# Kernel optimization log

Hardware: AMD Instinct MI355X
Metric: run time of the kernel (lower is better)

Reference implementation:

```python
import jax, jax.numpy as jnp
import numpy as np

N, E_RAND, IN, HID, OUT = 10000, 320000, 512, 256, 256
E = E_RAND + N  # random edges + self loops
TEMP, LAM, LAMBDA_LOSS, BN_EPS = 0.5, 1e-3, 1.0, 1e-5


def _normalize(x):
    # F.normalize: x / max(||x||, 1e-12)
    return x / jnp.maximum(jnp.linalg.norm(x, axis=-1, keepdims=True), 1e-12)


def setup_inputs() -> dict:
    key = jax.random.key(0)
    ks = jax.random.split(key, 12)
    feat = jax.random.normal(ks[0], (N, IN), jnp.float32)
    loops = jnp.arange(N)
    src = jnp.concatenate([jax.random.randint(ks[1], (E_RAND,), 0, N), loops])
    dst = jnp.concatenate([jax.random.randint(ks[2], (E_RAND,), 0, N), loops])
    def lin(k, i, o):
        return jax.random.normal(k, (i, o), jnp.float32) / np.sqrt(i).astype(np.float32)
    return {
        'feat': feat,
        'W1': lin(ks[3], IN, HID), 'b1': jnp.zeros((HID,), jnp.float32),
        'W2': lin(ks[4], HID, OUT), 'b2': jnp.zeros((OUT,), jnp.float32),
        'Wt1': lin(ks[5], IN, HID), 'bt1': jnp.zeros((HID,), jnp.float32),
        'gamma': jnp.ones((HID,), jnp.float32), 'beta': jnp.zeros((HID,), jnp.float32),
        'Wt2': lin(ks[6], HID, OUT), 'bt2': jnp.zeros((OUT,), jnp.float32),
        'Wp': lin(ks[7], HID, HID), 'bp': jnp.zeros((HID,), jnp.float32),
        'src': src, 'dst': dst,
    }


def reference(feat, W1, b1, W2, b2, Wt1, bt1, gamma, beta, Wt2, bt2, Wp, bp, src, dst):
    n = feat.shape[0]
    ones = jnp.ones(src.shape, feat.dtype)
    deg_out = jax.ops.segment_sum(ones, src, num_segments=n)
    deg_in = jax.ops.segment_sum(ones, dst, num_segments=n)
    # symmetric GCN norm per edge (self-loops included so degrees >= 1)
    norm_e = jax.lax.rsqrt(deg_out)[src] * jax.lax.rsqrt(deg_in)[dst]

    def gconv(x, W, b):
        xw = x @ W  # [n, d_out]
        agg = jax.ops.segment_sum(xw[src] * norm_e[:, None], dst, num_segments=n)
        return agg + b

    # GCN encoder (2 layers, no LN)
    h = jax.nn.relu(gconv(feat, W1, b1))
    h = gconv(h, W2, b2)

    # target MLP encoder: linear -> BN(train) -> relu -> linear
    t = feat @ Wt1 + bt1
    mu = t.mean(0)
    var = t.var(0)  # biased, as BatchNorm normalization
    t = (t - mu) * jax.lax.rsqrt(var + BN_EPS) * gamma + beta
    trans = jax.nn.relu(t) @ Wt2 + bt2

    z = _normalize(h)                    # [n, d]
    q = _normalize(trans @ Wp + bp)      # projector (num_MLP=1)

    # pos_score: per-edge sum(z[u]*q[v])/temp, mean over in-edges at v
    sim_e = jnp.einsum('ed,ed->e', z[src], q[dst]) / TEMP
    pos = jax.ops.segment_sum(sim_e, dst, num_segments=n) / deg_in

    # neg_score (neg_sample=0): dense NxN similarity row-sums
    neg_sim = jnp.exp(z @ z.T / TEMP).sum(1)           # per-node
    neg_sim2 = LAM * jnp.exp(z @ q.T / TEMP).sum(1)    # per-node
    m_e = jnp.log(neg_sim[dst] + neg_sim2[src])
    neg = jax.ops.segment_sum(m_e, dst, num_segments=n) / deg_in

    loss = jnp.mean(-pos + LAMBDA_LOSS * neg)
    return loss
```

## Files before the change

### kernel.cpp

```cpp
#include <hip/hip_runtime.h>
#include <stdint.h>


#define TEMP_INV 2.0f
#define LAMC 1.0e-3f
#define SSCALE 1.6986436f

typedef __attribute__((ext_vector_type(8))) __bf16 bf16x8;
typedef __attribute__((ext_vector_type(4))) float f32x4;

__device__ __forceinline__ unsigned short f2bf(float x) {
  union { float f; unsigned int u; } v; v.f = x;
  unsigned int r = v.u + 0x7FFFu + ((v.u >> 16) & 1u);
  return (unsigned short)(r >> 16);
}

__device__ __forceinline__ void g2lds16(const void* gc, void* l) {
  void* g = const_cast<void*>(gc);
  __builtin_amdgcn_global_load_lds(
      (__attribute__((address_space(1))) void*)g,
      (__attribute__((address_space(3))) void*)l, 16, 0, 0);
}

__global__ void k_deg(const int* __restrict__ src, const int* __restrict__ dst,
                      float* deg_out, float* deg_in, int E) {
  int i = blockIdx.x * blockDim.x + threadIdx.x;
  if (i < E) {
    atomicAdd(&deg_out[src[i]], 1.0f);
    atomicAdd(&deg_in[dst[i]], 1.0f);
  }
}

__global__ void k_rdeg(const float* __restrict__ deg_out, const float* __restrict__ deg_in,
                       float* rdo, float* rdi, float* idi, int N) {
  int i = blockIdx.x * blockDim.x + threadIdx.x;
  if (i < N) {
    float o = deg_out[i], d = deg_in[i];
    rdo[i] = rsqrtf(o);
    rdi[i] = rsqrtf(d);
    idi[i] = 1.0f / d;
  }
}

__global__ void k_scan(const float* __restrict__ deg, int* __restrict__ off, int N, int E) {
  __shared__ int sm[1024];
  int tid = threadIdx.x;
  int chunk = (N + 1023) / 1024;
  int b = tid * chunk;
  int sum = 0;
  for (int j = 0; j < chunk; j++) { int i = b + j; if (i < N) sum += (int)deg[i]; }
  sm[tid] = sum;
  __syncthreads();
  for (int s = 1; s < 1024; s <<= 1) {
    int v = (tid >= s) ? sm[tid - s] : 0;
    __syncthreads();
    sm[tid] += v;
    __syncthreads();
  }
  int run = (tid == 0) ? 0 : sm[tid - 1];
  for (int j = 0; j < chunk; j++) {
    int i = b + j;
    if (i < N) { off[i] = run; run += (int)deg[i]; }
  }
  if (tid == 0) off[N] = E;
}

__global__ void k_fill(const int* __restrict__ src, const int* __restrict__ dst,
                       const int* __restrict__ off, int* cur,
                       const float* __restrict__ rdo, const float* __restrict__ rdi,
                       int* adj, float* aw, int E) {
  int e = blockIdx.x * blockDim.x + threadIdx.x;
  if (e < E) {
    int u = src[e], v = dst[e];
    int slot = off[v] + atomicAdd(&cur[v], 1);
    adj[slot] = u;
    aw[slot] = rdo[u] * rdi[v];
  }
}

template <int K, bool BIAS>
__global__ __launch_bounds__(256, 2) void k_gemmL(const float* A,
                                                  const float* __restrict__ W,
                                                  const float* __restrict__ bias,
                                                  float* C, int M) {
  __shared__ __align__(1024) float Wl[2][32][256];
  const int tid = threadIdx.x;
  const int wv = tid >> 6, ln = tid & 63;
  const int rg = tid >> 4, cg = tid & 15;
  const int row0 = blockIdx.x * 32 + rg * 2;
  const int cb = cg * 4;
  int r0 = row0 < M ? row0 : M - 1;
  int r1 = row0 + 1 < M ? row0 + 1 : M - 1;
  const float* Ar0 = A + (size_t)r0 * K;
  const float* Ar1 = A + (size_t)r1 * K;

  auto STAGE = [&](int k0, int b) {
#pragma unroll
    for (int it = 0; it < 8; it++) {
      int r = it * 4 + wv;
      const float* g = W + (size_t)(k0 + r) * 256 + ln * 4;
      g2lds16(g, (char*)&Wl[b][r][0] + ln * 16);
    }
  };

  constexpr int NC = K / 32;
  STAGE(0, 0);
  float acc[2][16] = {};
  for (int t = 0; t < NC; t++) {
    __syncthreads();
    if (t + 1 < NC) STAGE((t + 1) * 32, (t + 1) & 1);
    const float* Wc = &Wl[t & 1][0][0];
    const int k0 = t * 32;
#pragma unroll
    for (int k4 = 0; k4 < 32; k4 += 4) {
      float4 a0 = *(const float4*)(Ar0 + k0 + k4);
      float4 a1 = *(const float4*)(Ar1 + k0 + k4);
      float a0v[4] = {a0.x, a0.y, a0.z, a0.w};
      float a1v[4] = {a1.x, a1.y, a1.z, a1.w};
#pragma unroll
      for (int i = 0; i < 4; i++) {
#pragma unroll
        for (int tt = 0; tt < 4; tt++) {
          float4 w4 = *(const float4*)(Wc + (k4 + i) * 256 + 64 * tt + cb);
          acc[0][4 * tt + 0] += a0v[i] * w4.x; acc[0][4 * tt + 1] += a0v[i] * w4.y;
          acc[0][4 * tt + 2] += a0v[i] * w4.z; acc[0][4 * tt + 3] += a0v[i] * w4.w;
          acc[1][4 * tt + 0] += a1v[i] * w4.x; acc[1][4 * tt + 1] += a1v[i] * w4.y;
          acc[1][4 * tt + 2] += a1v[i] * w4.z; acc[1][4 * tt + 3] += a1v[i] * w4.w;
        }
      }
    }
  }
#pragma unroll
  for (int r = 0; r < 2; r++) {
    int rr = row0 + r;
    if (rr < M) {
      float* crow = C + (size_t)rr * 256;
#pragma unroll
      for (int tt = 0; tt < 4; tt++) {
        int c = 64 * tt + cb;
        float4 v = {acc[r][4 * tt], acc[r][4 * tt + 1], acc[r][4 * tt + 2], acc[r][4 * tt + 3]};
        if constexpr (BIAS) {
          float4 b4 = *(const float4*)(bias + c);
          v.x += b4.x; v.y += b4.y; v.z += b4.z; v.w += b4.w;
        }
        *(float4*)(crow + c) = v;
      }
    }
  }
}

__global__ void k_bnstat(const float* __restrict__ T, float* s, float* ss, int M) {
  int c = threadIdx.x;
  int r0 = blockIdx.x * 64;
  float a = 0, b = 0;
  for (int r = r0; r < r0 + 64 && r < M; r++) {
    float v = T[(size_t)r * 256 + c];
    a += v; b += v * v;
  }
  atomicAdd(&s[c], a);
  atomicAdd(&ss[c], b);
}

__global__ void k_bnrelu(float* T, const float* __restrict__ s, const float* __restrict__ ss,
                         const float* __restrict__ g, const float* __restrict__ b, int M) {
  int r = blockIdx.x, c = threadIdx.x;
  float invM = 1.0f / (float)M;
  float mu = s[c] * invM;
  float var = ss[c] * invM - mu * mu;
  float w = rsqrtf(var + 1e-5f) * g[c];
  float v = T[(size_t)r * 256 + c];
  v = (v - mu) * w + b[c];
  T[(size_t)r * 256 + c] = fmaxf(v, 0.0f);
}

template <bool UNIT, bool RELU>
__global__ __launch_bounds__(256) void k_agg(const float* __restrict__ X, const int* __restrict__ off,
                                             const int* __restrict__ adj, const float* __restrict__ w,
                                             const float* __restrict__ bias, float* __restrict__ Y, int N) {
  int wv = threadIdx.x >> 6, ln = threadIdx.x & 63;
  int v = blockIdx.x * 4 + wv;
  if (v >= N) return;
  int s0 = off[v], s1 = off[v + 1];
  const float4* X4 = (const float4*)X;
  float4 acc = {0, 0, 0, 0};
  for (int s = s0; s < s1; s++) {
    int u = adj[s];
    float wt = UNIT ? 1.0f : w[s];
    float4 x = X4[(size_t)u * 64 + ln];
    acc.x += wt * x.x; acc.y += wt * x.y; acc.z += wt * x.z; acc.w += wt * x.w;
  }
  if constexpr (!UNIT) {
    float4 b = ((const float4*)bias)[ln];
    acc.x += b.x; acc.y += b.y; acc.z += b.z; acc.w += b.w;
  }
  if constexpr (RELU) {
    acc.x = fmaxf(acc.x, 0.f); acc.y = fmaxf(acc.y, 0.f);
    acc.z = fmaxf(acc.z, 0.f); acc.w = fmaxf(acc.w, 0.f);
  }
  ((float4*)Y)[(size_t)v * 64 + ln] = acc;
}

__global__ __launch_bounds__(256) void k_norm(float* X, unsigned short* Xb, int N, int NPAD) {
  int wv = threadIdx.x >> 6, ln = threadIdx.x & 63;
  int r = blockIdx.x * 4 + wv;
  if (r >= NPAD) return;
  if (r >= N) {
    ushort4 z = {0, 0, 0, 0};
    ((ushort4*)Xb)[(size_t)r * 64 + ln] = z;
    return;
  }
  float4 x = ((const float4*)X)[(size_t)r * 64 + ln];
  float ss = x.x * x.x + x.y * x.y + x.z * x.z + x.w * x.w;
#pragma unroll
  for (int m = 1; m < 64; m <<= 1) ss += __shfl_xor(ss, m, 64);
  float sc = 1.0f / fmaxf(sqrtf(ss), 1e-12f);
  float4 xn = {x.x * sc, x.y * sc, x.z * sc, x.w * sc};
  ((float4*)X)[(size_t)r * 64 + ln] = xn;
  float bs = sc * SSCALE;
  ushort4 b;
  b.x = f2bf(x.x * bs); b.y = f2bf(x.y * bs);
  b.z = f2bf(x.z * bs); b.w = f2bf(x.w * bs);
  ((ushort4*)Xb)[(size_t)r * 64 + ln] = b;
}

__global__ __launch_bounds__(256, 2) void k_sim(const unsigned short* __restrict__ Zb,
                                                const unsigned short* __restrict__ Qb,
                                                float* __restrict__ S1, float* __restrict__ S2,
                                                int N, int JT, int JS) {
  __shared__ __align__(1024) char LB[2][32768];
  const int tid = threadIdx.x;
  const int wv = tid >> 6, ln = tid & 63;
  const int i0 = blockIdx.x * 256;
  const int wb = wv * 64;

  auto STAGE = [&](int jt, int b) {
    int j0 = jt * 32;
    char* Lb = (char*)LB[b];
#pragma unroll
    for (int it = 0; it < 8; it++) {
      int c = it * 4 + wv;
      int L = c * 1024 + ln * 16;
      int r = L >> 9;
      int o = (L & 511) ^ ((r & 7) << 4);
      const char* g = (r < 32) ? (const char*)Zb + (size_t)(j0 + r) * 512 + o
                               : (const char*)Qb + (size_t)(j0 + r - 32) * 512 + o;
      g2lds16(g, Lb + c * 1024);
    }
  };

  int jt0 = (blockIdx.y * JT) / JS;
  int jt1 = ((blockIdx.y + 1) * JT) / JS;

  STAGE(jt0, 0);

  bf16x8 af[4][8];
#pragma unroll
  for (int rf = 0; rf < 4; rf++) {
    const char* arow = (const char*)(Zb + (size_t)(i0 + wb + rf * 16 + (ln & 15)) * 256);
#pragma unroll
    for (int kk = 0; kk < 8; kk++)
      af[rf][kk] = *(const bf16x8*)(arow + kk * 64 + ((ln >> 4) << 4));
  }

  f32x4 rs[4][2] = {};

  __syncthreads();
  int cur = 0;
  for (int jt = jt0; jt < jt1; jt++) {
    if (jt + 1 < jt1) STAGE(jt + 1, cur ^ 1);
    const char* Lb = (const char*)LB[cur];
#pragma unroll
    for (int m = 0; m < 2; m++) {
      f32x4 acc[4][2] = {};
#pragma unroll
      for (int kk = 0; kk < 8; kk++) {
#pragma unroll
        for (int cf = 0; cf < 2; cf++) {
          int brow = m * 32 + cf * 16 + (ln & 15);
          int o = (kk * 64 + ((ln >> 4) << 4)) ^ ((brow & 7) << 4);
          bf16x8 bb = *(const bf16x8*)(Lb + brow * 512 + o);
#pragma unroll
          for (int rf = 0; rf < 4; rf++)
            acc[rf][cf] = __builtin_amdgcn_mfma_f32_16x16x32_bf16(af[rf][kk], bb, acc[rf][cf], 0, 0, 0);
        }
      }
#pragma unroll
      for (int rf = 0; rf < 4; rf++)
#pragma unroll
        for (int i = 0; i < 4; i++)
          rs[rf][m][i] += exp2f(acc[rf][0][i]) + exp2f(acc[rf][1][i]);
    }
    __syncthreads();
    cur ^= 1;
  }

#pragma unroll
  for (int rf = 0; rf < 4; rf++)
#pragma unroll
    for (int m = 0; m < 2; m++)
#pragma unroll
      for (int i = 0; i < 4; i++) {
        float v = rs[rf][m][i];
        v += __shfl_xor(v, 1, 64);
        v += __shfl_xor(v, 2, 64);
        v += __shfl_xor(v, 4, 64);
        v += __shfl_xor(v, 8, 64);
        if ((ln & 15) == 0) {
          int row = i0 + wb + rf * 16 + ((ln >> 4) << 2) + i;
          if (row < N) atomicAdd(((m == 0) ? S1 : S2) + row, v);
        }
      }
}

__global__ __launch_bounds__(256) void k_final(const float* __restrict__ zsum, const float* __restrict__ q,
                                               const float* __restrict__ S1, const float* __restrict__ S2,
                                               const int* __restrict__ off, const int* __restrict__ adj,
                                               const float* __restrict__ idi, float* __restrict__ out,
                                               int N, float pad) {
  int wv = threadIdx.x >> 6, ln = threadIdx.x & 63;
  int v = blockIdx.x * 4 + wv;
  if (v >= N) return;
  float4 zs = ((const float4*)zsum)[(size_t)v * 64 + ln];
  float4 qv = ((const float4*)q)[(size_t)v * 64 + ln];
  float d = zs.x * qv.x + zs.y * qv.y + zs.z * qv.z + zs.w * qv.w;
  float s1v = S1[v] - pad;
  float lg = 0.0f;
  int e0 = off[v], e1 = off[v + 1];
  for (int s = e0 + ln; s < e1; s += 64) {
    int u = adj[s];
    lg += logf(s1v + LAMC * (S2[u] - pad));
  }
#pragma unroll
  for (int m = 1; m < 64; m <<= 1) {
    d += __shfl_xor(d, m, 64);
    lg += __shfl_xor(lg, m, 64);
  }
  if (ln == 0) {
    float inv = idi[v];
    float posv = d * inv * TEMP_INV;
    float negv = lg * inv;
    atomicAdd(out, (negv - posv) * (1.0f / (float)N));
  }
}

extern "C" void kernel_launch(void* const* d_in, const int* in_sizes, int n_in,
                              void* d_out, int out_size, void* d_ws, size_t ws_size,
                              hipStream_t stream) {
  const float* feat  = (const float*)d_in[0];
  const float* W1    = (const float*)d_in[1];
  const float* b1    = (const float*)d_in[2];
  const float* W2    = (const float*)d_in[3];
  const float* b2    = (const float*)d_in[4];
  const float* Wt1   = (const float*)d_in[5];
  const float* bt1   = (const float*)d_in[6];
  const float* gamma = (const float*)d_in[7];
  const float* beta  = (const float*)d_in[8];
  const float* Wt2   = (const float*)d_in[9];
  const float* bt2   = (const float*)d_in[10];
  const float* Wp    = (const float*)d_in[11];
  const float* bp    = (const float*)d_in[12];
  const int*   src   = (const int*)d_in[13];
  const int*   dst   = (const int*)d_in[14];
  const int N = in_sizes[0] / 512;
  const int E = in_sizes[13];
  const int NTI = (N + 255) / 256, NPAD = NTI * 256, JT = NPAD / 32;
  const int JS = 25;
  const float PADF = (float)(NPAD - N);

  char* p = (char*)d_ws;
  auto alloc = [&](size_t bytes) { char* r = p; p += (bytes + 255) & ~(size_t)255; return r; };
  float* B0 = (float*)alloc((size_t)N * 256 * 4);
  float* B1 = (float*)alloc((size_t)N * 256 * 4);
  float* B2 = (float*)alloc((size_t)N * 256 * 4);
  unsigned short* zb = (unsigned short*)alloc((size_t)NPAD * 256 * 2);
  unsigned short* qb = (unsigned short*)alloc((size_t)NPAD * 256 * 2);
  int*   off = (int*)alloc((size_t)(N + 1) * 4);
  int*   adj = (int*)alloc((size_t)E * 4);
  float* aw  = (float*)alloc((size_t)E * 4);
  char*  zblk = p;
  float* deg_out = (float*)alloc((size_t)N * 4);
  float* deg_in  = (float*)alloc((size_t)N * 4);
  int*   cur     = (int*)alloc((size_t)N * 4);
  float* S1 = (float*)alloc((size_t)N * 4);
  float* S2 = (float*)alloc((size_t)N * 4);
  float* bns  = (float*)alloc(256 * 4);
  float* bnss = (float*)alloc(256 * 4);
  size_t zbytes = (size_t)(p - zblk);
  float* rdo = (float*)alloc((size_t)N * 4);
  float* rdi = (float*)alloc((size_t)N * 4);
  float* idi = (float*)alloc((size_t)N * 4);
  (void)ws_size; (void)n_in; (void)out_size;

  hipMemsetAsync(zblk, 0, zbytes, stream);
  hipMemsetAsync(d_out, 0, 4, stream);

  int gE = (E + 255) / 256, gN = (N + 255) / 256, gb = (N + 31) / 32, gw = (N + 3) / 4;
  k_deg<<<gE, 256, 0, stream>>>(src, dst, deg_out, deg_in, E);
  k_rdeg<<<gN, 256, 0, stream>>>(deg_out, deg_in, rdo, rdi, idi, N);
  k_scan<<<1, 1024, 0, stream>>>(deg_in, off, N, E);
  k_fill<<<gE, 256, 0, stream>>>(src, dst, off, cur, rdo, rdi, adj, aw, E);

  k_gemmL<512, false><<<gb, 256, 0, stream>>>(feat, W1, nullptr, B0, N);
  k_gemmL<512, true ><<<gb, 256, 0, stream>>>(feat, Wt1, bt1, B1, N);
  k_bnstat<<<(N + 63) / 64, 256, 0, stream>>>(B1, bns, bnss, N);
  k_bnrelu<<<N, 256, 0, stream>>>(B1, bns, bnss, gamma, beta, N);
  k_gemmL<256, true ><<<gb, 256, 0, stream>>>(B1, Wt2, bt2, B1, N);
  k_gemmL<256, true ><<<gb, 256, 0, stream>>>(B1, Wp, bp, B1, N);

  k_agg<false, true ><<<gw, 256, 0, stream>>>(B0, off, adj, aw, b1, B2, N);
  k_gemmL<256, false><<<gb, 256, 0, stream>>>(B2, W2, nullptr, B0, N);
  k_agg<false, false><<<gw, 256, 0, stream>>>(B0, off, adj, aw, b2, B2, N);

  int gnp = (NPAD + 3) / 4;
  k_norm<<<gnp, 256, 0, stream>>>(B2, zb, N, NPAD);
  k_norm<<<gnp, 256, 0, stream>>>(B1, qb, N, NPAD);

  dim3 gs(NTI, JS);
  k_sim<<<gs, 256, 0, stream>>>(zb, qb, S1, S2, N, JT, JS);

  k_agg<true, false><<<gw, 256, 0, stream>>>(B2, off, adj, aw, nullptr, B0, N);
  k_final<<<gw, 256, 0, stream>>>(B0, B1, S1, S2, off, adj, idi, (float*)d_out, N, PADF);
}
```

Baseline: 814.0 us.

## Use split-bf16 MFMA for dense GEMMs and column-sliced edge aggregation

Replaces the fp32 FMA GEMM with an MFMA kernel. The kernel splits both A and W into bf16 high and low parts and accumulates three products (hi*hi, lo*hi, hi*lo) to keep near-fp32 accuracy. A new per-call kernel converts each weight matrix into transposed hi/lo bf16 buffers, which adds small extra launches. The sparse aggregation now gives each block a 64-column slice with a 4-way unrolled gather, which raises the number of blocks. It also adds s_setprio around the MFMA loops in k_sim and the new GEMM.

```diff
diff --git a/kernel.cpp b/kernel.cpp
--- a/kernel.cpp
+++ b/kernel.cpp
@@ -7,12 +7,16 @@
 #define SSCALE 1.6986436f
 
 typedef __attribute__((ext_vector_type(8))) __bf16 bf16x8;
+typedef __attribute__((ext_vector_type(8))) unsigned short u16x8;
 typedef __attribute__((ext_vector_type(4))) float f32x4;
 
 __device__ __forceinline__ unsigned short f2bf(float x) {
   union { float f; unsigned int u; } v; v.f = x;
   unsigned int r = v.u + 0x7FFFu + ((v.u >> 16) & 1u);
   return (unsigned short)(r >> 16);
+}
+__device__ __forceinline__ float bf2f(unsigned short h) {
+  union { unsigned int u; float f; } v; v.u = ((unsigned int)h) << 16; return v.f;
 }
 
 __device__ __forceinline__ void g2lds16(const void* gc, void* l) {
@@ -78,72 +82,92 @@
   }
 }
 
+__global__ void k_cvtWt(const float* __restrict__ W, unsigned short* __restrict__ Wth,
+                        unsigned short* __restrict__ Wtl, int K) {
+  int k = blockIdx.x, c = threadIdx.x;
+  float x = W[(size_t)k * 256 + c];
+  unsigned short h = f2bf(x);
+  Wth[(size_t)c * K + k] = h;
+  Wtl[(size_t)c * K + k] = f2bf(x - bf2f(h));
+}
+
 template <int K, bool BIAS>
-__global__ __launch_bounds__(256, 2) void k_gemmL(const float* A,
-                                                  const float* __restrict__ W,
-                                                  const float* __restrict__ bias,
-                                                  float* C, int M) {
-  __shared__ __align__(1024) float Wl[2][32][256];
-  const int tid = threadIdx.x;
-  const int wv = tid >> 6, ln = tid & 63;
-  const int rg = tid >> 4, cg = tid & 15;
-  const int row0 = blockIdx.x * 32 + rg * 2;
-  const int cb = cg * 4;
-  int r0 = row0 < M ? row0 : M - 1;
-  int r1 = row0 + 1 < M ? row0 + 1 : M - 1;
-  const float* Ar0 = A + (size_t)r0 * K;
-  const float* Ar1 = A + (size_t)r1 * K;
-
-  auto STAGE = [&](int k0, int b) {
+__global__ __launch_bounds__(256, 2) void k_gemmM(
+    const float* A,
+    const unsigned short* __restrict__ Wth, const unsigned short* __restrict__ Wtl,
+    const float* __restrict__ bias, float* C, int M) {
+  __shared__ __align__(1024) char LB[2][32768];
+  const int tid = threadIdx.x, wv = tid >> 6, ln = tid & 63;
+  const int rg = wv & 1, ch = wv >> 1;
+  const int i0 = blockIdx.x * 32;
+  int arow = i0 + rg * 16 + (ln & 15);
+  if (arow >= M) arow = M - 1;
+  const int kg = ln >> 4;
+  const float* Ar = A + (size_t)arow * K + kg * 8;
+
+  auto STAGE = [&](int kc, int b) {
 #pragma unroll
     for (int it = 0; it < 8; it++) {
-      int r = it * 4 + wv;
-      const float* g = W + (size_t)(k0 + r) * 256 + ln * 4;
-      g2lds16(g, (char*)&Wl[b][r][0] + ln * 16);
-    }
+      int idx = it * 4 + wv;
+      int mat = idx >> 4, s = (idx >> 2) & 3, cb = idx & 3;
+      const unsigned short* Wt = mat ? Wtl : Wth;
+      const char* src = (const char*)(Wt + (size_t)(cb * 64 + ln) * K) + kc * 64 + s * 16;
+      g2lds16(src, (char*)LB[b] + mat * 16384 + s * 4096 + cb * 1024);
+    }
+  };
+
+  auto LOADA = [&](int t, bf16x8& ah, bf16x8& al) {
+    float4 x0 = *(const float4*)(Ar + t * 32);
+    float4 x1 = *(const float4*)(Ar + t * 32 + 4);
+    float xs[8] = {x0.x, x0.y, x0.z, x0.w, x1.x, x1.y, x1.z, x1.w};
+    union { u16x8 u; bf16x8 b; } hu, lu;
+#pragma unroll
+    for (int j = 0; j < 8; j++) {
+      unsigned short h = f2bf(xs[j]);
+      hu.u[j] = h;
+      lu.u[j] = f2bf(xs[j] - bf2f(h));
+    }
+    ah = hu.b; al = lu.b;
   };
 
   constexpr int NC = K / 32;
   STAGE(0, 0);
-  float acc[2][16] = {};
+  bf16x8 ah, al;
+  LOADA(0, ah, al);
+  f32x4 acc[8] = {};
+  int b = 0;
+  __syncthreads();
   for (int t = 0; t < NC; t++) {
+    bf16x8 ah_n = ah, al_n = al;
+    if (t + 1 < NC) {
+      STAGE(t + 1, b ^ 1);
+      LOADA(t + 1, ah_n, al_n);
+    }
+    const char* Lb = (const char*)LB[b];
+    __builtin_amdgcn_s_setprio(1);
+#pragma unroll
+    for (int jf = 0; jf < 8; jf++) {
+      int col = ch * 128 + jf * 16 + (ln & 15);
+      bf16x8 bh = *(const bf16x8*)(Lb + kg * 4096 + col * 16);
+      bf16x8 bl = *(const bf16x8*)(Lb + 16384 + kg * 4096 + col * 16);
+      acc[jf] = __builtin_amdgcn_mfma_f32_16x16x32_bf16(ah, bh, acc[jf], 0, 0, 0);
+      acc[jf] = __builtin_amdgcn_mfma_f32_16x16x32_bf16(al, bh, acc[jf], 0, 0, 0);
+      acc[jf] = __builtin_amdgcn_mfma_f32_16x16x32_bf16(ah, bl, acc[jf], 0, 0, 0);
+    }
+    __builtin_amdgcn_s_setprio(0);
     __syncthreads();
-    if (t + 1 < NC) STAGE((t + 1) * 32, (t + 1) & 1);
-    const float* Wc = &Wl[t & 1][0][0];
-    const int k0 = t * 32;
-#pragma unroll
-    for (int k4 = 0; k4 < 32; k4 += 4) {
-      float4 a0 = *(const float4*)(Ar0 + k0 + k4);
-      float4 a1 = *(const float4*)(Ar1 + k0 + k4);
-      float a0v[4] = {a0.x, a0.y, a0.z, a0.w};
-      float a1v[4] = {a1.x, a1.y, a1.z, a1.w};
-#pragma unroll
-      for (int i = 0; i < 4; i++) {
-#pragma unroll
-        for (int tt = 0; tt < 4; tt++) {
-          float4 w4 = *(const float4*)(Wc + (k4 + i) * 256 + 64 * tt + cb);
-          acc[0][4 * tt + 0] += a0v[i] * w4.x; acc[0][4 * tt + 1] += a0v[i] * w4.y;
-          acc[0][4 * tt + 2] += a0v[i] * w4.z; acc[0][4 * tt + 3] += a0v[i] * w4.w;
-          acc[1][4 * tt + 0] += a1v[i] * w4.x; acc[1][4 * tt + 1] += a1v[i] * w4.y;
-          acc[1][4 * tt + 2] += a1v[i] * w4.z; acc[1][4 * tt + 3] += a1v[i] * w4.w;
-        }
-      }
-    }
-  }
-#pragma unroll
-  for (int r = 0; r < 2; r++) {
-    int rr = row0 + r;
-    if (rr < M) {
-      float* crow = C + (size_t)rr * 256;
-#pragma unroll
-      for (int tt = 0; tt < 4; tt++) {
-        int c = 64 * tt + cb;
-        float4 v = {acc[r][4 * tt], acc[r][4 * tt + 1], acc[r][4 * tt + 2], acc[r][4 * tt + 3]};
-        if constexpr (BIAS) {
-          float4 b4 = *(const float4*)(bias + c);
-          v.x += b4.x; v.y += b4.y; v.z += b4.z; v.w += b4.w;
-        }
-        *(float4*)(crow + c) = v;
+    b ^= 1; ah = ah_n; al = al_n;
+  }
+#pragma unroll
+  for (int i = 0; i < 4; i++) {
+    int row = i0 + rg * 16 + kg * 4 + i;
+    if (row < M) {
+#pragma unroll
+      for (int jf = 0; jf < 8; jf++) {
+        int col = ch * 128 + jf * 16 + (ln & 15);
+        float v = acc[jf][i];
+        if constexpr (BIAS) v += bias[col];
+        C[(size_t)row * 256 + col] = v;
       }
     }
   }
@@ -174,30 +198,32 @@
 }
 
 template <bool UNIT, bool RELU>
-__global__ __launch_bounds__(256) void k_agg(const float* __restrict__ X, const int* __restrict__ off,
-                                             const int* __restrict__ adj, const float* __restrict__ w,
-                                             const float* __restrict__ bias, float* __restrict__ Y, int N) {
+__global__ __launch_bounds__(256) void k_aggS(
+    const float* __restrict__ X, const int* __restrict__ off, const int* __restrict__ adj,
+    const float* __restrict__ w, const float* __restrict__ bias, float* __restrict__ Y,
+    int N, int NV) {
+  int slice = blockIdx.x / NV, vc = blockIdx.x - slice * NV;
   int wv = threadIdx.x >> 6, ln = threadIdx.x & 63;
-  int v = blockIdx.x * 4 + wv;
+  int v = vc * 4 + wv;
   if (v >= N) return;
+  int c = slice * 64 + ln;
   int s0 = off[v], s1 = off[v + 1];
-  const float4* X4 = (const float4*)X;
-  float4 acc = {0, 0, 0, 0};
-  for (int s = s0; s < s1; s++) {
-    int u = adj[s];
-    float wt = UNIT ? 1.0f : w[s];
-    float4 x = X4[(size_t)u * 64 + ln];
-    acc.x += wt * x.x; acc.y += wt * x.y; acc.z += wt * x.z; acc.w += wt * x.w;
-  }
-  if constexpr (!UNIT) {
-    float4 b = ((const float4*)bias)[ln];
-    acc.x += b.x; acc.y += b.y; acc.z += b.z; acc.w += b.w;
-  }
-  if constexpr (RELU) {
-    acc.x = fmaxf(acc.x, 0.f); acc.y = fmaxf(acc.y, 0.f);
-    acc.z = fmaxf(acc.z, 0.f); acc.w = fmaxf(acc.w, 0.f);
-  }
-  ((float4*)Y)[(size_t)v * 64 + ln] = acc;
+  float acc = 0.f;
+  int s = s0;
+  for (; s + 3 < s1; s += 4) {
+    int u0 = adj[s], u1 = adj[s + 1], u2 = adj[s + 2], u3 = adj[s + 3];
+    float x0 = X[(size_t)u0 * 256 + c], x1 = X[(size_t)u1 * 256 + c];
+    float x2 = X[(size_t)u2 * 256 + c], x3 = X[(size_t)u3 * 256 + c];
+    if constexpr (UNIT) acc += (x0 + x1) + (x2 + x3);
+    else acc += w[s] * x0 + w[s + 1] * x1 + w[s + 2] * x2 + w[s + 3] * x3;
+  }
+  for (; s < s1; s++) {
+    float wt = UNIT ? 1.f : w[s];
+    acc += wt * X[(size_t)adj[s] * 256 + c];
+  }
+  if constexpr (!UNIT) acc += bias[c];
+  if constexpr (RELU) acc = fmaxf(acc, 0.f);
+  Y[(size_t)v * 256 + c] = acc;
 }
 
 __global__ __launch_bounds__(256) void k_norm(float* X, unsigned short* Xb, int N, int NPAD) {
@@ -272,6 +298,7 @@
 #pragma unroll
     for (int m = 0; m < 2; m++) {
       f32x4 acc[4][2] = {};
+      __builtin_amdgcn_s_setprio(1);
 #pragma unroll
       for (int kk = 0; kk < 8; kk++) {
 #pragma unroll
@@ -284,6 +311,7 @@
             acc[rf][cf] = __builtin_amdgcn_mfma_f32_16x16x32_bf16(af[rf][kk], bb, acc[rf][cf], 0, 0, 0);
         }
       }
+      __builtin_amdgcn_s_setprio(0);
 #pragma unroll
       for (int rf = 0; rf < 4; rf++)
 #pragma unroll
@@ -374,6 +402,8 @@
   float* B2 = (float*)alloc((size_t)N * 256 * 4);
   unsigned short* zb = (unsigned short*)alloc((size_t)NPAD * 256 * 2);
   unsigned short* qb = (unsigned short*)alloc((size_t)NPAD * 256 * 2);
+  unsigned short* wth = (unsigned short*)alloc((size_t)256 * 512 * 2);
+  unsigned short* wtl = (unsigned short*)alloc((size_t)256 * 512 * 2);
   int*   off = (int*)alloc((size_t)(N + 1) * 4);
   int*   adj = (int*)alloc((size_t)E * 4);
   float* aw  = (float*)alloc((size_t)E * 4);
@@ -394,22 +424,30 @@
   hipMemsetAsync(zblk, 0, zbytes, stream);
   hipMemsetAsync(d_out, 0, 4, stream);
 
-  int gE = (E + 255) / 256, gN = (N + 255) / 256, gb = (N + 31) / 32, gw = (N + 3) / 4;
+  int gE = (E + 255) / 256, gN = (N + 255) / 256;
+  int NV = (N + 3) / 4, gw = NV, gm = (N + 31) / 32;
   k_deg<<<gE, 256, 0, stream>>>(src, dst, deg_out, deg_in, E);
   k_rdeg<<<gN, 256, 0, stream>>>(deg_out, deg_in, rdo, rdi, idi, N);
   k_scan<<<1, 1024, 0, stream>>>(deg_in, off, N, E);
   k_fill<<<gE, 256, 0, stream>>>(src, dst, off, cur, rdo, rdi, adj, aw, E);
 
-  k_gemmL<512, false><<<gb, 256, 0, stream>>>(feat, W1, nullptr, B0, N);
-  k_gemmL<512, true ><<<gb, 256, 0, stream>>>(feat, Wt1, bt1, B1, N);
+  k_cvtWt<<<512, 256, 0, stream>>>(W1, wth, wtl, 512);
+  k_gemmM<512, false><<<gm, 256, 0, stream>>>(feat, wth, wtl, nullptr, B0, N);
+  k_cvtWt<<<512, 256, 0, stream>>>(Wt1, wth, wtl, 512);
+  k_gemmM<512, true ><<<gm, 256, 0, stream>>>(feat, wth, wtl, bt1, B1, N);
+
   k_bnstat<<<(N + 63) / 64, 256, 0, stream>>>(B1, bns, bnss, N);
   k_bnrelu<<<N, 256, 0, stream>>>(B1, bns, bnss, gamma, beta, N);
-  k_gemmL<256, true ><<<gb, 256, 0, stream>>>(B1, Wt2, bt2, B1, N);
-  k_gemmL<256, true ><<<gb, 256, 0, stream>>>(B1, Wp, bp, B1, N);
-
-  k_agg<false, true ><<<gw, 256, 0, stream>>>(B0, off, adj, aw, b1, B2, N);
-  k_gemmL<256, false><<<gb, 256, 0, stream>>>(B2, W2, nullptr, B0, N);
-  k_agg<false, false><<<gw, 256, 0, stream>>>(B0, off, adj, aw, b2, B2, N);
+
+  k_cvtWt<<<256, 256, 0, stream>>>(Wt2, wth, wtl, 256);
+  k_gemmM<256, true ><<<gm, 256, 0, stream>>>(B1, wth, wtl, bt2, B1, N);
+  k_cvtWt<<<256, 256, 0, stream>>>(Wp, wth, wtl, 256);
+  k_gemmM<256, true ><<<gm, 256, 0, stream>>>(B1, wth, wtl, bp, B1, N);
+
+  k_aggS<false, true ><<<4 * gw, 256, 0, stream>>>(B0, off, adj, aw, b1, B2, N, NV);
+  k_cvtWt<<<256, 256, 0, stream>>>(W2, wth, wtl, 256);
+  k_gemmM<256, false><<<gm, 256, 0, stream>>>(B2, wth, wtl, nullptr, B0, N);
+  k_aggS<false, false><<<4 * gw, 256, 0, stream>>>(B0, off, adj, aw, b2, B2, N, NV);
 
   int gnp = (NPAD + 3) / 4;
   k_norm<<<gnp, 256, 0, stream>>>(B2, zb, N, NPAD);
@@ -418,6 +456,6 @@
   dim3 gs(NTI, JS);
   k_sim<<<gs, 256, 0, stream>>>(zb, qb, S1, S2, N, JT, JS);
 
-  k_agg<true, false><<<gw, 256, 0, stream>>>(B2, off, adj, aw, nullptr, B0, N);
+  k_aggS<true, false><<<4 * gw, 256, 0, stream>>>(B2, off, adj, aw, nullptr, B0, N, NV);
   k_final<<<gw, 256, 0, stream>>>(B0, B1, S1, S2, off, adj, idi, (float*)d_out, N, PADF);
 }
```

Result: faster. 781.6 us (-4.0%).
